# Performance work log

Measured on AMD Instinct MI355X. Metric: run time of the kernel, lower is better.

## Reference

```python
import jax, jax.numpy as jnp
import numpy as np

B, L, D = 8, 256, 64
N_USERS, N_LOCS, N_TIME = 10000, 50000, 169  # time index in 1..168 after (t-1)%168+1
EX_SU, EX_SL, EX_TU, EX_TL = 1.0, 0.0, 1.0, 0.0


def setup_inputs() -> dict:
    key = jax.random.key(0)
    ks = jax.random.split(key, 11)
    traj_input = jax.random.randint(ks[0], (B, L, 3), 0, N_USERS, dtype=jnp.int64)
    mat_input = jax.random.uniform(ks[1], (B, L, L, 2), dtype=jnp.float32)
    traj_length = jax.random.randint(ks[2], (B,), 1, L + 1, dtype=jnp.int64)
    s = 0.02
    emb_t = jax.random.normal(ks[3], (N_TIME, D), dtype=jnp.float32) * s
    emb_l = jax.random.normal(ks[4], (N_LOCS, D), dtype=jnp.float32) * s
    emb_u = jax.random.normal(ks[5], (N_USERS, D), dtype=jnp.float32) * s
    emb_su = jax.random.normal(ks[6], (2, D), dtype=jnp.float32) * s
    emb_sl = jax.random.normal(ks[7], (2, D), dtype=jnp.float32) * s
    emb_tu = jax.random.normal(ks[8], (2, D), dtype=jnp.float32) * s
    emb_tl = jax.random.normal(ks[9], (2, D), dtype=jnp.float32) * s
    return {"traj_input": traj_input, "mat_input": mat_input, "traj_length": traj_length,
            "emb_t": emb_t, "emb_l": emb_l, "emb_u": emb_u,
            "emb_su": emb_su, "emb_sl": emb_sl, "emb_tu": emb_tu, "emb_tl": emb_tl}


def reference(traj_input, mat_input, traj_length, emb_t, emb_l, emb_u,
              emb_su, emb_sl, emb_tu, emb_tl):
    hours = 24 * 7  # 168
    t_idx = (traj_input[:, :, 2] - 1) % hours + 1          # [B,L] in 1..168
    # joint embedding: three gathers fused into one add
    joint_embedding = emb_t[t_idx] + emb_l[traj_input[:, :, 1]] + emb_u[traj_input[:, :, 0]]  # [B,L,D]

    delta_spatial = mat_input[:, :, :, 0]                  # [B,L,L]
    delta_temporal = mat_input[:, :, :, 1]                 # [B,L,L]

    # mask[i, :len_i, :len_i] = 1, vectorized as an outer-AND of validity
    pos = jnp.arange(L)
    valid = pos[None, :] < traj_length[:, None]            # [B,L]
    mask = (valid[:, :, None] & valid[:, None, :]).astype(jnp.int32)  # [B,L,L] in {0,1}

    e_sl = emb_sl[mask]  # [B,L,L,D]
    e_su = emb_su[mask]
    e_tl = emb_tl[mask]
    e_tu = emb_tu[mask]

    v_sl = (delta_spatial - EX_SL)[..., None]              # broadcast instead of expand
    v_su = (EX_SU - delta_spatial)[..., None]
    v_tl = (delta_temporal - EX_TL)[..., None]
    v_tu = (EX_TU - delta_temporal)[..., None]

    spatial_interval = (e_sl * v_su + e_su * v_sl) / (EX_SU - EX_SL)
    temporal_interval = (e_tl * v_tu + e_tu * v_tl) / (EX_TU - EX_TL)
    delta_embedding = spatial_interval + temporal_interval  # [B,L,L,D]
    return joint_embedding, delta_embedding
```

## Files before the change

### kernel.cpp

```cpp
#include <hip/hip_runtime.h>


typedef float f4 __attribute__((ext_vector_type(4)));
typedef float f2 __attribute__((ext_vector_type(2)));

constexpr int HOURS   = 168;
constexpr int Dd      = 64;
constexpr int NJOINT4 = 8 * 256 * 64 / 4;
constexpr int NPAIR   = 8 * 256 * 256;
constexpr int NDELTA4 = NPAIR * Dd / 4;
constexpr int NTOT4   = NJOINT4 + NDELTA4;

__device__ __forceinline__ f4 ld4(const float* p) {
    return *reinterpret_cast<const f4*>(p);
}

__global__ __launch_bounds__(256) void ctr_fused_kernel(
    const int*   __restrict__ traj,
    const float* __restrict__ mat,
    const int*   __restrict__ lens,
    const float* __restrict__ emb_t,
    const float* __restrict__ emb_l,
    const float* __restrict__ emb_u,
    const float* __restrict__ emb_su,
    const float* __restrict__ emb_sl,
    const float* __restrict__ emb_tu,
    const float* __restrict__ emb_tl,
    float* __restrict__ out)
{
    __shared__ int s_len[8];

    const int tid = threadIdx.x;
    if (tid < 8) s_len[tid] = lens[tid];
    __syncthreads();

    const int tid_g = blockIdx.x * 256 + tid;
    const int dof = (tid_g & 15) * 4;

    f4 sl0 = ld4(emb_sl + dof), sl1 = ld4(emb_sl + 64 + dof);
    f4 su0 = ld4(emb_su + dof), su1 = ld4(emb_su + 64 + dof);
    f4 tl0 = ld4(emb_tl + dof), tl1 = ld4(emb_tl + 64 + dof);
    f4 tu0 = ld4(emb_tu + dof), tu1 = ld4(emb_tu + 64 + dof);

    const f4 base0 = sl0 + tl0, base1 = sl1 + tl1;
    const f4 cs0   = su0 - sl0, cs1   = su1 - sl1;
    const f4 ct0   = tu0 - tl0, ct1   = tu1 - tl1;

    const int stride = gridDim.x * 256;
    for (int g = tid_g; g < NTOT4; g += stride) {
        if (g < NJOINT4) {
            int row = g >> 4;
            int user = traj[row * 3 + 0];
            int loc  = traj[row * 3 + 1];
            int t    = traj[row * 3 + 2];
            int tm = (t - 1) % HOURS;
            if (tm < 0) tm += HOURS;
            int tx = tm + 1;
            f4 a = ld4(emb_t + tx * Dd + dof);
            f4 l = ld4(emb_l + loc * Dd + dof);
            f4 u = ld4(emb_u + user * Dd + dof);
            *reinterpret_cast<f4*>(&out[(size_t)g * 4]) = a + l + u;
        } else {
            int di   = g - NJOINT4;
            int pair = di >> 4;
            int b  = pair >> 16;
            int i  = (pair >> 8) & 255;
            int j  = pair & 255;
            int len = s_len[b];
            bool v = (i < len) && (j < len);
            f2 dd = *reinterpret_cast<const f2*>(&mat[(size_t)pair * 2]);
            f4 ba = v ? base1 : base0;
            f4 ca = v ? cs1   : cs0;
            f4 ta = v ? ct1   : ct0;
            f4 o = ba + dd.x * ca + dd.y * ta;
            *reinterpret_cast<f4*>(&out[(size_t)g * 4]) = o;
        }
    }
}

extern "C" void kernel_launch(void* const* d_in, const int* in_sizes, int n_in,
                              void* d_out, int out_size, void* d_ws, size_t ws_size,
                              hipStream_t stream) {
    const int*   traj   = (const int*)  d_in[0];
    const float* mat    = (const float*)d_in[1];
    const int*   lens   = (const int*)  d_in[2];
    const float* emb_t  = (const float*)d_in[3];
    const float* emb_l  = (const float*)d_in[4];
    const float* emb_u  = (const float*)d_in[5];
    const float* emb_su = (const float*)d_in[6];
    const float* emb_sl = (const float*)d_in[7];
    const float* emb_tu = (const float*)d_in[8];
    const float* emb_tl = (const float*)d_in[9];
    float* out = (float*)d_out;

    ctr_fused_kernel<<<2048, 256, 0, stream>>>(
        traj, mat, lens, emb_t, emb_l, emb_u, emb_su, emb_sl, emb_tu, emb_tl, out);
}
```

Baseline: 29.07 us.

## Assign contiguous per-wave chunks for delta output and split joint work by wave

Replaces the grid-stride loop with a fixed mapping: each wavefront handles a contiguous chunk of 2048 float4 delta outputs in an unrolled loop, and the first waves also compute one joint-embedding float4 each. The per-element branch, shared-memory length staging and its __syncthreads are removed, with the length loaded once per wave since a chunk never crosses a batch boundary. The grid is halved to 1024 blocks. This cuts loop and branch overhead and allows more memory operations in flight, but relies on the exact problem sizes matching the hardcoded chunking.

```diff
diff --git a/kernel.cpp b/kernel.cpp
--- a/kernel.cpp
+++ b/kernel.cpp
@@ -7,9 +7,9 @@
 constexpr int HOURS   = 168;
 constexpr int Dd      = 64;
 constexpr int NJOINT4 = 8 * 256 * 64 / 4;
-constexpr int NPAIR   = 8 * 256 * 256;
-constexpr int NDELTA4 = NPAIR * Dd / 4;
-constexpr int NTOT4   = NJOINT4 + NDELTA4;
+constexpr int NJOINT  = NJOINT4 * 4;
+constexpr int PER_WAVE = 2048;
+constexpr int ITERS    = PER_WAVE / 64;
 
 __device__ __forceinline__ f4 ld4(const float* p) {
     return *reinterpret_cast<const f4*>(p);
@@ -28,53 +28,51 @@
     const float* __restrict__ emb_tl,
     float* __restrict__ out)
 {
-    __shared__ int s_len[8];
+    const int tid  = threadIdx.x;
+    const int wave = blockIdx.x * 4 + (tid >> 6);
+    const int lane = tid & 63;
+    const int g0   = wave * PER_WAVE + lane;
+    const int d4f  = (lane & 15) * 4;
 
-    const int tid = threadIdx.x;
-    if (tid < 8) s_len[tid] = lens[tid];
-    __syncthreads();
-
-    const int tid_g = blockIdx.x * 256 + tid;
-    const int dof = (tid_g & 15) * 4;
-
-    f4 sl0 = ld4(emb_sl + dof), sl1 = ld4(emb_sl + 64 + dof);
-    f4 su0 = ld4(emb_su + dof), su1 = ld4(emb_su + 64 + dof);
-    f4 tl0 = ld4(emb_tl + dof), tl1 = ld4(emb_tl + 64 + dof);
-    f4 tu0 = ld4(emb_tu + dof), tu1 = ld4(emb_tu + 64 + dof);
-
+    f4 sl0 = ld4(emb_sl + d4f), sl1 = ld4(emb_sl + 64 + d4f);
+    f4 su0 = ld4(emb_su + d4f), su1 = ld4(emb_su + 64 + d4f);
+    f4 tl0 = ld4(emb_tl + d4f), tl1 = ld4(emb_tl + 64 + d4f);
+    f4 tu0 = ld4(emb_tu + d4f), tu1 = ld4(emb_tu + 64 + d4f);
     const f4 base0 = sl0 + tl0, base1 = sl1 + tl1;
     const f4 cs0   = su0 - sl0, cs1   = su1 - sl1;
     const f4 ct0   = tu0 - tl0, ct1   = tu1 - tl1;
 
-    const int stride = gridDim.x * 256;
-    for (int g = tid_g; g < NTOT4; g += stride) {
-        if (g < NJOINT4) {
-            int row = g >> 4;
-            int user = traj[row * 3 + 0];
-            int loc  = traj[row * 3 + 1];
-            int t    = traj[row * 3 + 2];
-            int tm = (t - 1) % HOURS;
-            if (tm < 0) tm += HOURS;
-            int tx = tm + 1;
-            f4 a = ld4(emb_t + tx * Dd + dof);
-            f4 l = ld4(emb_l + loc * Dd + dof);
-            f4 u = ld4(emb_u + user * Dd + dof);
-            *reinterpret_cast<f4*>(&out[(size_t)g * 4]) = a + l + u;
-        } else {
-            int di   = g - NJOINT4;
-            int pair = di >> 4;
-            int b  = pair >> 16;
-            int i  = (pair >> 8) & 255;
-            int j  = pair & 255;
-            int len = s_len[b];
-            bool v = (i < len) && (j < len);
-            f2 dd = *reinterpret_cast<const f2*>(&mat[(size_t)pair * 2]);
-            f4 ba = v ? base1 : base0;
-            f4 ca = v ? cs1   : cs0;
-            f4 ta = v ? ct1   : ct0;
-            f4 o = ba + dd.x * ca + dd.y * ta;
-            *reinterpret_cast<f4*>(&out[(size_t)g * 4]) = o;
-        }
+    if (wave < NJOINT4 / 64) {
+        int jidx = wave * 64 + lane;
+        int row  = jidx >> 4;
+        int user = traj[row * 3 + 0];
+        int loc  = traj[row * 3 + 1];
+        int t    = traj[row * 3 + 2];
+        int tm = (t - 1) % HOURS;
+        if (tm < 0) tm += HOURS;
+        int tx = tm + 1;
+        f4 o = ld4(emb_t + tx * Dd + d4f)
+             + ld4(emb_l + loc * Dd + d4f)
+             + ld4(emb_u + user * Dd + d4f);
+        *reinterpret_cast<f4*>(&out[(size_t)jidx * 4]) = o;
+    }
+
+    const int b   = g0 >> 20;
+    const int len = lens[b];
+
+#pragma unroll 8
+    for (int k = 0; k < ITERS; ++k) {
+        int idx  = g0 + k * 64;
+        int pair = idx >> 4;
+        int i    = (pair >> 8) & 255;
+        int j    = pair & 255;
+        bool v   = (i < len) && (j < len);
+        f2 dd = *reinterpret_cast<const f2*>(&mat[(size_t)pair * 2]);
+        f4 ba = v ? base1 : base0;
+        f4 ca = v ? cs1   : cs0;
+        f4 ta = v ? ct1   : ct0;
+        f4 o = ba + dd.x * ca + dd.y * ta;
+        *reinterpret_cast<f4*>(&out[NJOINT + (size_t)idx * 4]) = o;
     }
 }
 
@@ -93,6 +91,6 @@
     const float* emb_tl = (const float*)d_in[9];
     float* out = (float*)d_out;
 
-    ctr_fused_kernel<<<2048, 256, 0, stream>>>(
+    ctr_fused_kernel<<<1024, 256, 0, stream>>>(
         traj, mat, lens, emb_t, emb_l, emb_u, emb_su, emb_sl, emb_tu, emb_tl, out);
 }
```

After: 28.21 us. 2.9% less time.

## Prefetch all mat values up front and unroll fixed delta iterations per thread

Applied to the files above, without the earlier changes.

The grid-stride loop becomes a fixed 16-iteration unrolled loop. All mat pair values are loaded into registers before the joint-embedding gather so the memory loads overlap. The small interval embeddings are combined once per block in shared memory instead of each thread loading them from global memory. The joint part is handled once by the first threads, and the loop relies on a hardcoded grid size of 2048 blocks times 256 threads, which raises register use.

```diff
diff --git a/kernel.cpp b/kernel.cpp
--- a/kernel.cpp
+++ b/kernel.cpp
@@ -7,9 +7,9 @@
 constexpr int HOURS   = 168;
 constexpr int Dd      = 64;
 constexpr int NJOINT4 = 8 * 256 * 64 / 4;
-constexpr int NPAIR   = 8 * 256 * 256;
-constexpr int NDELTA4 = NPAIR * Dd / 4;
-constexpr int NTOT4   = NJOINT4 + NDELTA4;
+constexpr int NJOINT  = NJOINT4 * 4;
+constexpr int STRIDE4 = 524288;
+constexpr int KITERS  = 16;
 
 __device__ __forceinline__ f4 ld4(const float* p) {
     return *reinterpret_cast<const f4*>(p);
@@ -28,53 +28,63 @@
     const float* __restrict__ emb_tl,
     float* __restrict__ out)
 {
-    __shared__ int s_len[8];
+    __shared__ float s_base[2][64], s_cs[2][64], s_ct[2][64];
+    __shared__ int   s_len[8];
 
     const int tid = threadIdx.x;
+    if (tid < 128) {
+        int m = tid >> 6, d = tid & 63;
+        float sl = emb_sl[tid], su = emb_su[tid];
+        float tl = emb_tl[tid], tu = emb_tu[tid];
+        s_base[m][d] = sl + tl;
+        s_cs[m][d]   = su - sl;
+        s_ct[m][d]   = tu - tl;
+    }
     if (tid < 8) s_len[tid] = lens[tid];
+
+    const int tid_g = blockIdx.x * 256 + tid;
+    const int dof   = (tid_g & 15) * 4;
+
+    f2 dd[KITERS];
+#pragma unroll
+    for (int k = 0; k < KITERS; ++k) {
+        int pair = (tid_g + k * STRIDE4) >> 4;
+        dd[k] = *reinterpret_cast<const f2*>(&mat[(size_t)pair * 2]);
+    }
+
+    if (tid_g < NJOINT4) {
+        int row  = tid_g >> 4;
+        int user = traj[row * 3 + 0];
+        int loc  = traj[row * 3 + 1];
+        int t    = traj[row * 3 + 2];
+        int tm = (t - 1) % HOURS;
+        if (tm < 0) tm += HOURS;
+        int tx = tm + 1;
+        f4 o = ld4(emb_t + tx * Dd + dof)
+             + ld4(emb_l + loc * Dd + dof)
+             + ld4(emb_u + user * Dd + dof);
+        *reinterpret_cast<f4*>(&out[(size_t)tid_g * 4]) = o;
+    }
+
     __syncthreads();
 
-    const int tid_g = blockIdx.x * 256 + tid;
-    const int dof = (tid_g & 15) * 4;
+    const f4 base0 = ld4(&s_base[0][dof]), base1 = ld4(&s_base[1][dof]);
+    const f4 cs0   = ld4(&s_cs[0][dof]),   cs1   = ld4(&s_cs[1][dof]);
+    const f4 ct0   = ld4(&s_ct[0][dof]),   ct1   = ld4(&s_ct[1][dof]);
 
-    f4 sl0 = ld4(emb_sl + dof), sl1 = ld4(emb_sl + 64 + dof);
-    f4 su0 = ld4(emb_su + dof), su1 = ld4(emb_su + 64 + dof);
-    f4 tl0 = ld4(emb_tl + dof), tl1 = ld4(emb_tl + 64 + dof);
-    f4 tu0 = ld4(emb_tu + dof), tu1 = ld4(emb_tu + 64 + dof);
-
-    const f4 base0 = sl0 + tl0, base1 = sl1 + tl1;
-    const f4 cs0   = su0 - sl0, cs1   = su1 - sl1;
-    const f4 ct0   = tu0 - tl0, ct1   = tu1 - tl1;
-
-    const int stride = gridDim.x * 256;
-    for (int g = tid_g; g < NTOT4; g += stride) {
-        if (g < NJOINT4) {
-            int row = g >> 4;
-            int user = traj[row * 3 + 0];
-            int loc  = traj[row * 3 + 1];
-            int t    = traj[row * 3 + 2];
-            int tm = (t - 1) % HOURS;
-            if (tm < 0) tm += HOURS;
-            int tx = tm + 1;
-            f4 a = ld4(emb_t + tx * Dd + dof);
-            f4 l = ld4(emb_l + loc * Dd + dof);
-            f4 u = ld4(emb_u + user * Dd + dof);
-            *reinterpret_cast<f4*>(&out[(size_t)g * 4]) = a + l + u;
-        } else {
-            int di   = g - NJOINT4;
-            int pair = di >> 4;
-            int b  = pair >> 16;
-            int i  = (pair >> 8) & 255;
-            int j  = pair & 255;
-            int len = s_len[b];
-            bool v = (i < len) && (j < len);
-            f2 dd = *reinterpret_cast<const f2*>(&mat[(size_t)pair * 2]);
-            f4 ba = v ? base1 : base0;
-            f4 ca = v ? cs1   : cs0;
-            f4 ta = v ? ct1   : ct0;
-            f4 o = ba + dd.x * ca + dd.y * ta;
-            *reinterpret_cast<f4*>(&out[(size_t)g * 4]) = o;
-        }
+#pragma unroll
+    for (int k = 0; k < KITERS; ++k) {
+        int di   = tid_g + k * STRIDE4;
+        int pair = di >> 4;
+        int b  = pair >> 16;
+        int i  = (pair >> 8) & 255;
+        int j  = pair & 255;
+        int len = s_len[b];
+        bool v = (i < len) && (j < len);
+        f4 o = (v ? base1 : base0)
+             + dd[k].x * (v ? cs1 : cs0)
+             + dd[k].y * (v ? ct1 : ct0);
+        *reinterpret_cast<f4*>(&out[NJOINT + (size_t)di * 4]) = o;
     }
 }
 
```

Result: no change. 28.88 us (-0.6%).
